# Kernel optimization log

Measured on AMD Instinct MI355X. Metric: run time of the kernel, lower is better.

Reference implementation:

```python
import jax, jax.numpy as jnp
import numpy as np

B, CIN, H, W = 256, 1280, 7, 7
A, NCLS, HID, NGT = 9, 20, 128, 40
OUT_DIM = 5 * A + NCLS  # 65


def setup_inputs() -> dict:
    key = jax.random.key(0)
    ks = jax.random.split(key, 8)
    features = jax.random.normal(ks[0], (B, CIN, H, W), jnp.float32)
    # grid: (x, y) centers of each feature cell, in feature-map coordinates
    grid = jax.random.uniform(ks[1], (B, H, W, 2), jnp.float32) * 7.0
    # GT boxes (x1, y1, x2, y2, class), padded count NGT per image
    xy1 = jax.random.uniform(ks[2], (B, NGT, 2), jnp.float32) * 5.0
    wh = jax.random.uniform(ks[3], (B, NGT, 2), jnp.float32) * 2.0 + 0.5
    cls = jax.random.randint(ks[4], (B, NGT, 1), 0, NCLS).astype(jnp.float32)
    bboxes = jnp.concatenate([xy1, xy1 + wh, cls], axis=-1)
    # anchor shapes (w, h) as in SingleStageDetector.__init__
    anc = jnp.array([[1.0, 1], [2, 2], [3, 3], [4, 4], [5, 5],
                     [2, 3], [3, 2], [3, 5], [5, 3]], jnp.float32)
    W1 = jax.random.normal(ks[5], (HID, CIN), jnp.float32) * 0.02
    b1 = jnp.zeros((HID,), jnp.float32)
    W2 = jax.random.normal(ks[6], (OUT_DIM, HID), jnp.float32) * 0.02
    b2 = jnp.zeros((OUT_DIM,), jnp.float32)
    return dict(features=features, grid=grid, bboxes=bboxes, anc=anc,
                W1=W1, b1=b1, W2=W2, b2=b2)


def reference(features, grid, bboxes, anc, W1, b1, W2, b2):
    Bx = features.shape[0]
    # --- PredictionNetwork (inference mode; dropout is identity at eval) ---
    h = jnp.einsum('bchw,oc->bohw', features, W1) + b1[None, :, None, None]
    h = jax.nn.leaky_relu(h, negative_slope=0.01)
    out = jnp.einsum('bchw,oc->bohw', h, W2) + b2[None, :, None, None]
    conf_scores = jax.nn.sigmoid(out[:, 4 * A:5 * A])          # (B, A, H, W)
    offsets = out[:, :4 * A].reshape(Bx, A, 4, H, W)
    offsets = jnp.concatenate(
        [jax.nn.sigmoid(offsets[:, :, :2]) - 0.5, offsets[:, :, 2:]], axis=2)
    class_scores = out[:, 5 * A:]                               # (B, C, H, W)
    # --- GenerateAnchor: (B, A, H, W, 4) as (x_tl, y_tl, x_br, y_br) ---
    ctr = grid[:, None]                    # (B, 1, H, W, 2)
    half = anc[None, :, None, None, :] / 2  # (1, A, 1, 1, 2)
    anchors = jnp.concatenate([ctr - half, ctr + half], axis=-1)
    # --- IoU: (B, A*H*W, N) ---
    P = anchors.reshape(Bx, -1, 4)          # (B, AHW, 4)
    gt = bboxes[..., :4]                    # (B, N, 4)
    tl = jnp.maximum(P[:, :, None, :2], gt[:, None, :, :2])
    br = jnp.minimum(P[:, :, None, 2:], gt[:, None, :, 2:])
    inter = jnp.prod(jnp.clip(br - tl, 0.0), axis=-1)  # (B, AHW, N)
    # torch code zeroes intersections for proposals with any coord <= 0
    legal = (jnp.min(P, axis=-1) > 0)[..., None]
    inter = inter * legal
    p_area = ((P[:, :, 2] - P[:, :, 0]) * (P[:, :, 3] - P[:, :, 1]))[:, :, None]
    g_area = ((gt[:, :, 2] - gt[:, :, 0]) * (gt[:, :, 3] - gt[:, :, 1]))[:, None, :]
    iou_mat = inter / (g_area + p_area - inter)
    return (conf_scores, offsets, class_scores, iou_mat)
```

## Files before the change

### kernel.cpp

```cpp
#include <hip/hip_runtime.h>


#define CIN_  1280
#define HW_   49
#define HID_  128
#define OUTD_ 65
#define NGT_  40
#define NP_   441
#define NCH   20

#define CONF_OFF 0
#define OFFS_OFF 112896
#define CLS_OFF  564480
#define IOU_OFF  815360

#define W1C_U32  81920

typedef __bf16 bf16x8 __attribute__((ext_vector_type(8)));
typedef float  f32x4  __attribute__((ext_vector_type(4)));

__device__ __forceinline__ unsigned pack2bf(float lo, float hi) {
    unsigned a = __float_as_uint(lo);
    unsigned b = __float_as_uint(hi);
    a = (a + 0x7FFFu + ((a >> 16) & 1u)) >> 16;
    b = (b + 0x7FFFu + ((b >> 16) & 1u)) >> 16;
    return a | (b << 16);
}
__device__ __forceinline__ float bflo(unsigned u) { return __uint_as_float(u << 16); }
__device__ __forceinline__ float bfhi(unsigned u) { return __uint_as_float(u & 0xFFFF0000u); }
__device__ __forceinline__ float sigmoidf_(float v) { return 1.f / (1.f + __expf(-v)); }

__device__ __forceinline__ bf16x8 ld_frag(const unsigned* p) {
    union { uint4 u; bf16x8 v; } x;
    x.u = *(const uint4*)p;
    return x.v;
}
__device__ __forceinline__ void gld_lds16(const unsigned* g, unsigned* l) {
    __builtin_amdgcn_global_load_lds(
        (const __attribute__((address_space(1))) unsigned*)g,
        (__attribute__((address_space(3))) unsigned*)l, 16, 0, 0);
}

__global__ __launch_bounds__(256) void prep_w1(const float* __restrict__ W1,
                                               unsigned* __restrict__ gW1c) {
    int X = blockIdx.x * 256 + threadIdx.x;
    int ch = X >> 12;
    int Xc = X & 4095;
    int o  = Xc >> 5;
    int phys_blk = (Xc >> 2) & 7;
    int win = Xc & 3;
    int blk = phys_blk ^ (o & 7);
    int cp  = blk * 4 + win;
    int c   = ch * 64 + 2 * cp;
    float2 f = *(const float2*)(W1 + o * CIN_ + c);
    gW1c[X] = pack2bf(f.x, f.y);
}

__global__ __launch_bounds__(512) void fused_kernel(
    const float* __restrict__ F,
    const float* __restrict__ grid,
    const float* __restrict__ bbox,
    const float* __restrict__ anc,
    const unsigned* __restrict__ gW1c,
    const float* __restrict__ B1,
    const float* __restrict__ W2,
    const float* __restrict__ B2,
    float* __restrict__ out)
{
    __shared__ unsigned lds[14144];
    unsigned* smA = lds;
    unsigned* smB = lds + 8192;
    unsigned* smH = lds + 11008;
    float* smP = (float*)lds;
    float* smG = (float*)(lds + 4096);

    const int tid  = threadIdx.x;
    const int b    = blockIdx.x;
    const int lane = tid & 63;
    const int w    = tid >> 6;
    const int quad = lane >> 4;
    const int m16  = lane & 15;

    const float* Fb = F + b * (CIN_ * HW_);

    const int cps = tid >> 4;
    const int hwb = tid & 15;

    f32x4 acc[4];
    #pragma unroll
    for (int nt = 0; nt < 4; ++nt) acc[nt] = (f32x4)(0.f);

    float fb0[4], fb1[4];

    {
        const unsigned* g = gW1c + (w * 2) * 256 + lane * 4;
        unsigned* l = smA + (w * 2) * 256;
        gld_lds16(g, l);
        gld_lds16(g + 256, l + 256);
        #pragma unroll
        for (int s = 0; s < 4; ++s) {
            int hw = hwb + 16 * s;
            if (hw < HW_) {
                const float* src = Fb + (2 * cps) * HW_ + hw;
                fb0[s] = src[0]; fb1[s] = src[HW_];
            }
        }
    }
    __syncthreads();
    #pragma unroll
    for (int s = 0; s < 4; ++s) {
        int hw = hwb + 16 * s;
        if (hw < HW_) smB[hw * 44 + cps] = pack2bf(fb0[s], fb1[s]);
    }
    __syncthreads();

    const int swz = (m16 & 7);
    for (int ch = 0; ch < NCH; ++ch) {
        const int p = ch & 1;
        if (ch < NCH - 1) {
            const unsigned* g = gW1c + (ch + 1) * 4096 + (w * 2) * 256 + lane * 4;
            unsigned* l = smA + (p ^ 1) * 4096 + (w * 2) * 256;
            gld_lds16(g, l);
            gld_lds16(g + 256, l + 256);
            const int c0n = (ch + 1) * 64;
            #pragma unroll
            for (int s = 0; s < 4; ++s) {
                int hw = hwb + 16 * s;
                if (hw < HW_) {
                    const float* src = Fb + (c0n + 2 * cps) * HW_ + hw;
                    fb0[s] = src[0]; fb1[s] = src[HW_];
                }
            }
        }
        {
            const unsigned* Ab = smA + p * 4096 + ((w * 16 + m16) << 5);
            bf16x8 a0 = ld_frag(Ab + ((quad ^ swz) << 2));
            bf16x8 a1 = ld_frag(Ab + (((4 + quad) ^ swz) << 2));
            const unsigned* Bb = smB + m16 * 44 + quad * 4;
            #pragma unroll
            for (int nt = 0; nt < 4; ++nt) {
                bf16x8 b0 = ld_frag(Bb + nt * 16 * 44);
                bf16x8 b1 = ld_frag(Bb + nt * 16 * 44 + 16);
                acc[nt] = __builtin_amdgcn_mfma_f32_16x16x32_bf16(a0, b0, acc[nt], 0, 0, 0);
                acc[nt] = __builtin_amdgcn_mfma_f32_16x16x32_bf16(a1, b1, acc[nt], 0, 0, 0);
            }
        }
        __syncthreads();
        if (ch < NCH - 1) {
            #pragma unroll
            for (int s = 0; s < 4; ++s) {
                int hw = hwb + 16 * s;
                if (hw < HW_) smB[hw * 44 + cps] = pack2bf(fb0[s], fb1[s]);
            }
        }
        __syncthreads();
    }

    #pragma unroll
    for (int nt = 0; nt < 4; ++nt) {
        int hw = nt * 16 + m16;
        if (hw < HW_) {
            #pragma unroll
            for (int rp = 0; rp < 2; ++rp) {
                int o0 = w * 16 + quad * 4 + 2 * rp;
                float v0 = acc[nt][2 * rp]     + B1[o0];
                float v1 = acc[nt][2 * rp + 1] + B1[o0 + 1];
                v0 = v0 > 0.f ? v0 : 0.01f * v0;
                v1 = v1 > 0.f ? v1 : 0.01f * v1;
                smH[(o0 >> 1) * HW_ + hw] = pack2bf(v0, v1);
            }
        }
    }

    if (tid < NP_) {
        int pp = tid, a = pp / 49, r = pp - a * 49;
        float cx = grid[b * 98 + 2 * r], cy = grid[b * 98 + 2 * r + 1];
        float hx = anc[2 * a] * 0.5f,    hy = anc[2 * a + 1] * 0.5f;
        float x1 = cx - hx, y1 = cy - hy, x2 = cx + hx, y2 = cy + hy;
        smP[pp * 6 + 0] = x1; smP[pp * 6 + 1] = y1;
        smP[pp * 6 + 2] = x2; smP[pp * 6 + 3] = y2;
        smP[pp * 6 + 4] = (x2 - x1) * (y2 - y1);
        smP[pp * 6 + 5] = (fminf(fminf(x1, y1), fminf(x2, y2)) > 0.f) ? 1.f : 0.f;
    }
    if (tid >= 472) {
        int g = tid - 472;
        float x1 = bbox[b * 200 + g * 5 + 0];
        float y1 = bbox[b * 200 + g * 5 + 1];
        float x2 = bbox[b * 200 + g * 5 + 2];
        float y2 = bbox[b * 200 + g * 5 + 3];
        smG[g * 5 + 0] = x1; smG[g * 5 + 1] = y1;
        smG[g * 5 + 2] = x2; smG[g * 5 + 3] = y2;
        smG[g * 5 + 4] = (x2 - x1) * (y2 - y1);
    }
    __syncthreads();

    for (int idx = tid; idx < OUTD_ * HW_; idx += 512) {
        int o2 = idx / 49;
        int hw = idx - o2 * 49;
        const float2* wr = (const float2*)(W2 + o2 * HID_);
        float s0 = 0.f, s1 = 0.f;
        #pragma unroll 8
        for (int k2 = 0; k2 < 64; ++k2) {
            unsigned hp = smH[k2 * HW_ + hw];
            float2 wv = wr[k2];
            s0 = fmaf(wv.x, bflo(hp), s0);
            s1 = fmaf(wv.y, bfhi(hp), s1);
        }
        float a = B2[o2] + (s0 + s1);

        unsigned int dst;
        float val;
        if (o2 < 36) {
            int an = o2 >> 2, kk = o2 & 3;
            val = (kk < 2) ? (sigmoidf_(a) - 0.5f) : a;
            dst = OFFS_OFF + b * 1764 + an * 196 + kk * 49 + hw;
        } else if (o2 < 45) {
            val = sigmoidf_(a);
            dst = CONF_OFF + b * 441 + (o2 - 36) * 49 + hw;
        } else {
            val = a;
            dst = CLS_OFF + b * 980 + (o2 - 45) * 49 + hw;
        }
        out[dst] = val;
    }

    for (int idx = tid; idx < NP_ * NGT_; idx += 512) {
        int pp = idx / 40;
        int g  = idx - pp * 40;
        const float* P = smP + pp * 6;
        const float* G = smG + g * 5;
        float tlx = fmaxf(P[0], G[0]);
        float tly = fmaxf(P[1], G[1]);
        float brx = fminf(P[2], G[2]);
        float bry = fminf(P[3], G[3]);
        float dx = fmaxf(brx - tlx, 0.f);
        float dy = fmaxf(bry - tly, 0.f);
        float inter = dx * dy * P[5];
        out[IOU_OFF + b * (NP_ * NGT_) + idx] = inter / (G[4] + P[4] - inter);
    }
}

__global__ __launch_bounds__(512) void fused_fallback(
    const float* __restrict__ F, const float* __restrict__ grid,
    const float* __restrict__ bbox, const float* __restrict__ anc,
    const float* __restrict__ W1, const float* __restrict__ B1,
    const float* __restrict__ W2, const float* __restrict__ B2,
    float* __restrict__ out)
{
    __shared__ unsigned lds[4608 + 2304 + 6272];
    unsigned* smA = lds;
    unsigned* smB = lds + 4608;
    float*    smH = (float*)(lds + 4608 + 2304);
    float* smP = (float*)lds;
    float* smG = (float*)(lds + 4608);

    const int tid  = threadIdx.x;
    const int b    = blockIdx.x;
    const int lane = tid & 63;
    const int w    = tid >> 6;
    const int quad = lane >> 4;
    const int m16  = lane & 15;
    const float* Fb = F + b * (CIN_ * HW_);

    f32x4 acc[4];
    #pragma unroll
    for (int nt = 0; nt < 4; ++nt) acc[nt] = (f32x4)(0.f);

    for (int ch = 0; ch < NCH; ++ch) {
        const int c0 = ch * 64;
        __syncthreads();
        #pragma unroll
        for (int rr = 0; rr < 8; ++rr) {
            int pi = tid + rr * 512;
            int o = pi >> 5, cp = pi & 31;
            float2 f = *(const float2*)(F , (const float2*)nullptr == nullptr ?
                        (const float2*)( ( (const float*)0 ) ) : (const float2*)0), ff;
            (void)f; (void)ff;
            float2 fx = *(const float2*)(((const float*)W1) + o * CIN_ + c0 + 2 * cp);
            smA[o * 36 + cp] = pack2bf(fx.x, fx.y);
        }
        for (int pi = tid; pi < 32 * 49; pi += 512) {
            int cp = pi / 49;
            int hw = pi - cp * 49;
            const float* src = Fb + (c0 + 2 * cp) * HW_ + hw;
            smB[hw * 36 + cp] = pack2bf(src[0], src[HW_]);
        }
        __syncthreads();
        const unsigned* Ab = smA + (w * 16 + m16) * 36 + quad * 4;
        const unsigned* Bb = smB + m16 * 36 + quad * 4;
        #pragma unroll
        for (int ks = 0; ks < 2; ++ks) {
            bf16x8 af = ld_frag(Ab + ks * 16);
            #pragma unroll
            for (int nt = 0; nt < 4; ++nt) {
                bf16x8 bf = ld_frag(Bb + nt * 16 * 36 + ks * 16);
                acc[nt] = __builtin_amdgcn_mfma_f32_16x16x32_bf16(af, bf, acc[nt], 0, 0, 0);
            }
        }
    }
    #pragma unroll
    for (int nt = 0; nt < 4; ++nt) {
        int hw = nt * 16 + m16;
        if (hw < HW_) {
            #pragma unroll
            for (int r = 0; r < 4; ++r) {
                int o = w * 16 + quad * 4 + r;
                float v = acc[nt][r] + B1[o];
                v = v > 0.f ? v : 0.01f * v;
                smH[o * HW_ + hw] = v;
            }
        }
    }
    __syncthreads();
    if (tid < NP_) {
        int pp = tid, a = pp / 49, r = pp - a * 49;
        float cx = grid[b * 98 + 2 * r], cy = grid[b * 98 + 2 * r + 1];
        float hx = anc[2 * a] * 0.5f,    hy = anc[2 * a + 1] * 0.5f;
        float x1 = cx - hx, y1 = cy - hy, x2 = cx + hx, y2 = cy + hy;
        smP[pp * 6 + 0] = x1; smP[pp * 6 + 1] = y1;
        smP[pp * 6 + 2] = x2; smP[pp * 6 + 3] = y2;
        smP[pp * 6 + 4] = (x2 - x1) * (y2 - y1);
        smP[pp * 6 + 5] = (fminf(fminf(x1, y1), fminf(x2, y2)) > 0.f) ? 1.f : 0.f;
    }
    if (tid >= 472) {
        int g = tid - 472;
        float x1 = bbox[b * 200 + g * 5 + 0];
        float y1 = bbox[b * 200 + g * 5 + 1];
        float x2 = bbox[b * 200 + g * 5 + 2];
        float y2 = bbox[b * 200 + g * 5 + 3];
        smG[g * 5 + 0] = x1; smG[g * 5 + 1] = y1;
        smG[g * 5 + 2] = x2; smG[g * 5 + 3] = y2;
        smG[g * 5 + 4] = (x2 - x1) * (y2 - y1);
    }
    for (int idx = tid; idx < OUTD_ * HW_; idx += 512) {
        int o2 = idx / 49;
        int hw = idx - o2 * 49;
        const float4* wr = (const float4*)(W2 + o2 * HID_);
        const float*  hc = smH + hw;
        float s0 = 0.f, s1 = 0.f, s2 = 0.f, s3 = 0.f;
        #pragma unroll 8
        for (int k4 = 0; k4 < 32; ++k4) {
            float4 wv = wr[k4];
            s0 = fmaf(wv.x, hc[(4 * k4 + 0) * HW_], s0);
            s1 = fmaf(wv.y, hc[(4 * k4 + 1) * HW_], s1);
            s2 = fmaf(wv.z, hc[(4 * k4 + 2) * HW_], s2);
            s3 = fmaf(wv.w, hc[(4 * k4 + 3) * HW_], s3);
        }
        float a = B2[o2] + ((s0 + s1) + (s2 + s3));
        unsigned int dst; float val;
        if (o2 < 36) { int an = o2 >> 2, kk = o2 & 3;
            val = (kk < 2) ? (sigmoidf_(a) - 0.5f) : a;
            dst = OFFS_OFF + b * 1764 + an * 196 + kk * 49 + hw;
        } else if (o2 < 45) { val = sigmoidf_(a);
            dst = CONF_OFF + b * 441 + (o2 - 36) * 49 + hw;
        } else { val = a;
            dst = CLS_OFF + b * 980 + (o2 - 45) * 49 + hw; }
        out[dst] = val;
    }
    __syncthreads();
    for (int idx = tid; idx < NP_ * NGT_; idx += 512) {
        int pp = idx / 40;
        int g  = idx - pp * 40;
        const float* P = smP + pp * 6;
        const float* G = smG + g * 5;
        float tlx = fmaxf(P[0], G[0]);
        float tly = fmaxf(P[1], G[1]);
        float brx = fminf(P[2], G[2]);
        float bry = fminf(P[3], G[3]);
        float dx = fmaxf(brx - tlx, 0.f);
        float dy = fmaxf(bry - tly, 0.f);
        float inter = dx * dy * P[5];
        out[IOU_OFF + b * (NP_ * NGT_) + idx] = inter / (G[4] + P[4] - inter);
    }
}

extern "C" void kernel_launch(void* const* d_in, const int* in_sizes, int n_in,
                              void* d_out, int out_size, void* d_ws, size_t ws_size,
                              hipStream_t stream) {
    const float* F  = (const float*)d_in[0];
    const float* G  = (const float*)d_in[1];
    const float* BB = (const float*)d_in[2];
    const float* AN = (const float*)d_in[3];
    const float* W1 = (const float*)d_in[4];
    const float* B1 = (const float*)d_in[5];
    const float* W2 = (const float*)d_in[6];
    const float* B2 = (const float*)d_in[7];
    float* out = (float*)d_out;

    if (ws_size >= (size_t)W1C_U32 * 4) {
        unsigned* gW1c = (unsigned*)d_ws;
        prep_w1<<<320, 256, 0, stream>>>(W1, gW1c);
        fused_kernel<<<256, 512, 0, stream>>>(F, G, BB, AN, gW1c, B1, W2, B2, out);
    } else {
        fused_fallback<<<256, 512, 0, stream>>>(F, G, BB, AN, W1, B1, W2, B2, out);
    }
}
```

Measured before the change: 149.0 us.

## Stage whole feature map in LDS and stream W1 fragments directly to registers

Loads the entire per-image feature tile (1280 channels × 49 positions, packed to bf16) into LDS once up front, instead of double-buffering 64-channel chunks with two barriers per chunk. W1 is pre-packed into the exact MFMA fragment layout so each wave loads its A fragments straight from global memory into registers, prefetched one chunk ahead. The fourth N-tile now reuses a valid row and keeps only position 48, so no out-of-range rows are read. This removes all per-chunk barriers, but the up-front load is no longer overlapped with compute and the block needs about 126 KB of LDS, which limits occupancy to one block per CU.

```diff
diff --git a/kernel.cpp b/kernel.cpp
--- a/kernel.cpp
+++ b/kernel.cpp
@@ -14,7 +14,10 @@
 #define CLS_OFF  564480
 #define IOU_OFF  815360
 
-#define W1C_U32  81920
+#define W1F_U32  81920
+
+#define SF_STRIDE 644
+#define SF_SIZE   (49 * SF_STRIDE)
 
 typedef __bf16 bf16x8 __attribute__((ext_vector_type(8)));
 typedef float  f32x4  __attribute__((ext_vector_type(4)));
@@ -35,25 +38,23 @@
     x.u = *(const uint4*)p;
     return x.v;
 }
-__device__ __forceinline__ void gld_lds16(const unsigned* g, unsigned* l) {
-    __builtin_amdgcn_global_load_lds(
-        (const __attribute__((address_space(1))) unsigned*)g,
-        (__attribute__((address_space(3))) unsigned*)l, 16, 0, 0);
+__device__ __forceinline__ bf16x8 as_bf(uint4 u) {
+    union { uint4 u; bf16x8 v; } x; x.u = u; return x.v;
 }
 
 __global__ __launch_bounds__(256) void prep_w1(const float* __restrict__ W1,
-                                               unsigned* __restrict__ gW1c) {
+                                               unsigned* __restrict__ gW1f) {
     int X = blockIdx.x * 256 + threadIdx.x;
-    int ch = X >> 12;
-    int Xc = X & 4095;
-    int o  = Xc >> 5;
-    int phys_blk = (Xc >> 2) & 7;
-    int win = Xc & 3;
-    int blk = phys_blk ^ (o & 7);
-    int cp  = blk * 4 + win;
-    int c   = ch * 64 + 2 * cp;
+    int sub  = X & 3;
+    int lane = (X >> 2) & 63;
+    int r    = X >> 8;
+    int ks   = r & 1;
+    int w    = (r >> 1) & 7;
+    int ch   = r >> 4;
+    int o = w * 16 + (lane & 15);
+    int c = ch * 64 + ks * 32 + (lane >> 4) * 8 + sub * 2;
     float2 f = *(const float2*)(W1 + o * CIN_ + c);
-    gW1c[X] = pack2bf(f.x, f.y);
+    gW1f[X] = pack2bf(f.x, f.y);
 }
 
 __global__ __launch_bounds__(512) void fused_kernel(
@@ -61,18 +62,17 @@
     const float* __restrict__ grid,
     const float* __restrict__ bbox,
     const float* __restrict__ anc,
-    const unsigned* __restrict__ gW1c,
+    const unsigned* __restrict__ gW1f,
     const float* __restrict__ B1,
     const float* __restrict__ W2,
     const float* __restrict__ B2,
     float* __restrict__ out)
 {
-    __shared__ unsigned lds[14144];
-    unsigned* smA = lds;
-    unsigned* smB = lds + 8192;
-    unsigned* smH = lds + 11008;
-    float* smP = (float*)lds;
-    float* smG = (float*)(lds + 4096);
+    __shared__ unsigned lds[SF_SIZE];
+    unsigned* smF = lds;
+    unsigned* smH = lds;
+    float* smP = (float*)(lds + 3136);
+    float* smG = (float*)(lds + 3136 + 2646);
 
     const int tid  = threadIdx.x;
     const int b    = blockIdx.x;
@@ -83,83 +83,55 @@
 
     const float* Fb = F + b * (CIN_ * HW_);
 
-    const int cps = tid >> 4;
-    const int hwb = tid & 15;
+    for (int i = tid; i < 640 * 49; i += 512) {
+        int cp = i / 49;
+        int hw = i - cp * 49;
+        const float* s = Fb + (2 * cp) * HW_ + hw;
+        smF[hw * SF_STRIDE + cp] = pack2bf(s[0], s[HW_]);
+    }
+    __syncthreads();
+
+    const int row3 = (m16 == 0) ? 48 : (m16 - 1);
+    const unsigned* Bb[4] = {
+        smF + (0 * 16 + m16) * SF_STRIDE + quad * 4,
+        smF + (1 * 16 + m16) * SF_STRIDE + quad * 4,
+        smF + (2 * 16 + m16) * SF_STRIDE + quad * 4,
+        smF + row3 * SF_STRIDE + quad * 4
+    };
+
+    const uint4* Aw = (const uint4*)gW1f + (w * 2) * 64 + lane;
 
     f32x4 acc[4];
     #pragma unroll
     for (int nt = 0; nt < 4; ++nt) acc[nt] = (f32x4)(0.f);
 
-    float fb0[4], fb1[4];
-
-    {
-        const unsigned* g = gW1c + (w * 2) * 256 + lane * 4;
-        unsigned* l = smA + (w * 2) * 256;
-        gld_lds16(g, l);
-        gld_lds16(g + 256, l + 256);
+    uint4 a0 = Aw[0];
+    uint4 a1 = Aw[64];
+    for (int ch = 0; ch < NCH; ++ch) {
+        uint4 na0, na1;
+        if (ch < NCH - 1) {
+            na0 = Aw[(ch + 1) * 1024];
+            na1 = Aw[(ch + 1) * 1024 + 64];
+        }
+        const int coff = ch * 32;
+        bf16x8 aa0 = as_bf(a0);
+        bf16x8 aa1 = as_bf(a1);
         #pragma unroll
-        for (int s = 0; s < 4; ++s) {
-            int hw = hwb + 16 * s;
-            if (hw < HW_) {
-                const float* src = Fb + (2 * cps) * HW_ + hw;
-                fb0[s] = src[0]; fb1[s] = src[HW_];
-            }
-        }
-    }
-    __syncthreads();
-    #pragma unroll
-    for (int s = 0; s < 4; ++s) {
-        int hw = hwb + 16 * s;
-        if (hw < HW_) smB[hw * 44 + cps] = pack2bf(fb0[s], fb1[s]);
-    }
-    __syncthreads();
-
-    const int swz = (m16 & 7);
-    for (int ch = 0; ch < NCH; ++ch) {
-        const int p = ch & 1;
-        if (ch < NCH - 1) {
-            const unsigned* g = gW1c + (ch + 1) * 4096 + (w * 2) * 256 + lane * 4;
-            unsigned* l = smA + (p ^ 1) * 4096 + (w * 2) * 256;
-            gld_lds16(g, l);
-            gld_lds16(g + 256, l + 256);
-            const int c0n = (ch + 1) * 64;
-            #pragma unroll
-            for (int s = 0; s < 4; ++s) {
-                int hw = hwb + 16 * s;
-                if (hw < HW_) {
-                    const float* src = Fb + (c0n + 2 * cps) * HW_ + hw;
-                    fb0[s] = src[0]; fb1[s] = src[HW_];
-                }
-            }
-        }
-        {
-            const unsigned* Ab = smA + p * 4096 + ((w * 16 + m16) << 5);
-            bf16x8 a0 = ld_frag(Ab + ((quad ^ swz) << 2));
-            bf16x8 a1 = ld_frag(Ab + (((4 + quad) ^ swz) << 2));
-            const unsigned* Bb = smB + m16 * 44 + quad * 4;
-            #pragma unroll
-            for (int nt = 0; nt < 4; ++nt) {
-                bf16x8 b0 = ld_frag(Bb + nt * 16 * 44);
-                bf16x8 b1 = ld_frag(Bb + nt * 16 * 44 + 16);
-                acc[nt] = __builtin_amdgcn_mfma_f32_16x16x32_bf16(a0, b0, acc[nt], 0, 0, 0);
-                acc[nt] = __builtin_amdgcn_mfma_f32_16x16x32_bf16(a1, b1, acc[nt], 0, 0, 0);
-            }
-        }
-        __syncthreads();
-        if (ch < NCH - 1) {
-            #pragma unroll
-            for (int s = 0; s < 4; ++s) {
-                int hw = hwb + 16 * s;
-                if (hw < HW_) smB[hw * 44 + cps] = pack2bf(fb0[s], fb1[s]);
-            }
-        }
-        __syncthreads();
-    }
+        for (int nt = 0; nt < 4; ++nt) {
+            bf16x8 b0 = ld_frag(Bb[nt] + coff);
+            bf16x8 b1 = ld_frag(Bb[nt] + coff + 16);
+            acc[nt] = __builtin_amdgcn_mfma_f32_16x16x32_bf16(aa0, b0, acc[nt], 0, 0, 0);
+            acc[nt] = __builtin_amdgcn_mfma_f32_16x16x32_bf16(aa1, b1, acc[nt], 0, 0, 0);
+        }
+        a0 = na0; a1 = na1;
+    }
+
+    __syncthreads();
 
     #pragma unroll
     for (int nt = 0; nt < 4; ++nt) {
-        int hw = nt * 16 + m16;
-        if (hw < HW_) {
+        int hw = (nt < 3) ? (nt * 16 + m16) : ((m16 == 0) ? 48 : -1);
+        if (hw >= 0) {
             #pragma unroll
             for (int rp = 0; rp < 2; ++rp) {
                 int o0 = w * 16 + quad * 4 + 2 * rp;
@@ -273,10 +245,7 @@
         for (int rr = 0; rr < 8; ++rr) {
             int pi = tid + rr * 512;
             int o = pi >> 5, cp = pi & 31;
-            float2 f = *(const float2*)(F , (const float2*)nullptr == nullptr ?
-                        (const float2*)( ( (const float*)0 ) ) : (const float2*)0), ff;
-            (void)f; (void)ff;
-            float2 fx = *(const float2*)(((const float*)W1) + o * CIN_ + c0 + 2 * cp);
+            float2 fx = *(const float2*)(W1 + o * CIN_ + c0 + 2 * cp);
             smA[o * 36 + cp] = pack2bf(fx.x, fx.y);
         }
         for (int pi = tid; pi < 32 * 49; pi += 512) {
@@ -387,10 +356,10 @@
     const float* B2 = (const float*)d_in[7];
     float* out = (float*)d_out;
 
-    if (ws_size >= (size_t)W1C_U32 * 4) {
-        unsigned* gW1c = (unsigned*)d_ws;
-        prep_w1<<<320, 256, 0, stream>>>(W1, gW1c);
-        fused_kernel<<<256, 512, 0, stream>>>(F, G, BB, AN, gW1c, B1, W2, B2, out);
+    if (ws_size >= (size_t)W1F_U32 * 4) {
+        unsigned* gW1f = (unsigned*)d_ws;
+        prep_w1<<<320, 256, 0, stream>>>(W1, gW1f);
+        fused_kernel<<<256, 512, 0, stream>>>(F, G, BB, AN, gW1f, B1, W2, B2, out);
     } else {
         fused_fallback<<<256, 512, 0, stream>>>(F, G, BB, AN, W1, B1, W2, B2, out);
     }
```

Result: faster. 141.3 us (-5.2%).
